# Kernel optimization log

Hardware: AMD Instinct MI355X
Metric: run time of the kernel (lower is better)

Reference implementation:

```python
import jax, jax.numpy as jnp
import numpy as np

B, DIM, HEADS, H, W = 4, 192, 6, 256, 256
C = DIM // HEADS  # channels per head
DN = ('NCHW', 'OIHW', 'NCHW')


def conv2d(x, w, b, padding='VALID', groups=1):
    y = jax.lax.conv_general_dilated(x, w, (1, 1), padding,
                                     dimension_numbers=DN,
                                     feature_group_count=groups)
    return y + b[None, :, None, None]


def setup_inputs() -> dict:
    key = jax.random.key(0)
    ks = jax.random.split(key, 8)
    s = 0.02
    return {
        'x': jax.random.normal(ks[0], (B, DIM, H, W), jnp.float32),
        'qkv_w': jax.random.normal(ks[1], (3 * DIM, DIM, 1, 1), jnp.float32) * s,
        'qkv_b': jnp.zeros((3 * DIM,), jnp.float32),
        'dw_w': jax.random.normal(ks[2], (3 * DIM, 1, 3, 3), jnp.float32) * s,
        'dw_b': jnp.zeros((3 * DIM,), jnp.float32),
        'proj_w': jax.random.normal(ks[3], (DIM, DIM, 1, 1), jnp.float32) * s,
        'proj_b': jnp.zeros((DIM,), jnp.float32),
        'temperature': jnp.ones((HEADS, 1, 1, 1), jnp.float32),
    }


def reference(x, qkv_w, qkv_b, dw_w, dw_b, proj_w, proj_b, temperature):
    # qkv projection: 1x1 conv then 3x3 depthwise conv
    qkv = conv2d(x, qkv_w, qkv_b)
    qkv = conv2d(qkv, dw_w, dw_b, padding='SAME', groups=3 * DIM)
    q, k, v = jnp.split(qkv, 3, axis=1)  # each (B, DIM, H, W)

    def heads(t):
        return t.reshape(B, HEADS, C, H, W)
    q, k, v = heads(q), heads(k), heads(v)

    # L2-normalize along W (matches F.normalize eps=1e-12)
    eps = 1e-12
    q = q / jnp.maximum(jnp.linalg.norm(q, axis=-1, keepdims=True), eps)
    k = k / jnp.maximum(jnp.linalg.norm(k, axis=-1, keepdims=True), eps)

    # per-channel HxH attention, contraction over W; temperature broadcasts over head
    attn = jnp.einsum('bncxw,bncyw->bncxy', q, k) * temperature  # (B,HEADS,C,H,H)
    attn = jax.nn.softmax(attn, axis=-1)
    out = jnp.einsum('bncxy,bncyw->bncxw', attn, v)  # (B,HEADS,C,H,W)

    out = out.reshape(B, DIM, H, W)
    return conv2d(out, proj_w, proj_b)
```

## Files before the change

### kernel.cpp

```cpp
#include <hip/hip_runtime.h>
#include <hip/hip_bf16.h>
#include <math.h>


#define HW 65536
#define IMW 256

typedef short bf16x8 __attribute__((ext_vector_type(8)));
typedef float f32x4  __attribute__((ext_vector_type(4)));

__device__ __forceinline__ float bf2f(ushort u) {
    return __uint_as_float((uint)u << 16);
}
__device__ __forceinline__ ushort f2bf(float f) {
    uint i = __float_as_uint(f);
    return (ushort)((i + 0x7FFFu + ((i >> 16) & 1u)) >> 16);
}

__global__ __launch_bounds__(256) void cvt_f32_bf16(const float* __restrict__ s,
                                                    ushort* __restrict__ d, int n)
{
    int i = blockIdx.x * 256 + threadIdx.x;
    if (i < n) d[i] = f2bf(s[i]);
}

__global__ __launch_bounds__(256) void cvt_transpose_f32(const float* __restrict__ src,
                                                         ushort* __restrict__ dst,
                                                         int R, int C,
                                                         long ssS, long ssD)
{
    __shared__ ushort Ls[64][72];
    int t = threadIdx.x;
    long z = blockIdx.z;
    src += z * ssS; dst += z * ssD;
    int c0 = blockIdx.x * 64, r0 = blockIdx.y * 64;
    {
        int r = t >> 2, cs = t & 3;
        const float* gp = src + (size_t)(r0 + r) * C + c0 + cs * 16;
        ushort tmp[16];
        #pragma unroll
        for (int q = 0; q < 4; ++q) {
            float4 v = *(const float4*)(gp + q * 4);
            tmp[q*4+0] = f2bf(v.x); tmp[q*4+1] = f2bf(v.y);
            tmp[q*4+2] = f2bf(v.z); tmp[q*4+3] = f2bf(v.w);
        }
        *(uint4*)&Ls[r][cs * 16]     = *(uint4*)&tmp[0];
        *(uint4*)&Ls[r][cs * 16 + 8] = *(uint4*)&tmp[8];
    }
    __syncthreads();
    {
        int cc = t & 63, seg = t >> 6;
        ushort tmp[16];
        #pragma unroll
        for (int j = 0; j < 16; ++j) tmp[j] = Ls[seg * 16 + j][cc];
        ushort* op = dst + (size_t)(c0 + cc) * R + r0 + seg * 16;
        *(uint4*)(op)     = *(uint4*)&tmp[0];
        *(uint4*)(op + 8) = *(uint4*)&tmp[8];
    }
}

__global__ __launch_bounds__(256) void transpose_bf16(const ushort* __restrict__ src,
                                                      ushort* __restrict__ dst,
                                                      int R, int C,
                                                      long ssS, long ssD)
{
    __shared__ ushort Ls[64][72];
    int t = threadIdx.x;
    long z = blockIdx.z;
    src += z * ssS; dst += z * ssD;
    int c0 = blockIdx.x * 64, r0 = blockIdx.y * 64;
    {
        int r = t >> 2, cs = t & 3;
        const ushort* gp = src + (size_t)(r0 + r) * C + c0 + cs * 16;
        *(uint4*)&Ls[r][cs * 16]     = *(const uint4*)(gp);
        *(uint4*)&Ls[r][cs * 16 + 8] = *(const uint4*)(gp + 8);
    }
    __syncthreads();
    {
        int cc = t & 63, seg = t >> 6;
        ushort tmp[16];
        #pragma unroll
        for (int j = 0; j < 16; ++j) tmp[j] = Ls[seg * 16 + j][cc];
        ushort* op = dst + (size_t)(c0 + cc) * R + r0 + seg * 16;
        *(uint4*)(op)     = *(uint4*)&tmp[0];
        *(uint4*)(op + 8) = *(uint4*)&tmp[8];
    }
}

__global__ __launch_bounds__(256) void transpose_v(const ushort* __restrict__ post,
                                                   ushort* __restrict__ vt)
{
    __shared__ ushort Ls[64][72];
    int t = threadIdx.x;
    int s = blockIdx.z;
    int b = s / 192, r = s - b * 192;
    const ushort* src = post + ((size_t)b * 576 + 384 + r) * HW;
    ushort*       dst = vt + (size_t)s * HW;
    int c0 = blockIdx.x * 64, r0 = blockIdx.y * 64;
    {
        int rr = t >> 2, cs = t & 3;
        const ushort* gp = src + (size_t)(r0 + rr) * IMW + c0 + cs * 16;
        *(uint4*)&Ls[rr][cs * 16]     = *(const uint4*)(gp);
        *(uint4*)&Ls[rr][cs * 16 + 8] = *(const uint4*)(gp + 8);
    }
    __syncthreads();
    {
        int cc = t & 63, seg = t >> 6;
        ushort tmp[16];
        #pragma unroll
        for (int j = 0; j < 16; ++j) tmp[j] = Ls[seg * 16 + j][cc];
        ushort* op = dst + (size_t)(c0 + cc) * IMW + r0 + seg * 16;
        *(uint4*)(op)     = *(uint4*)&tmp[0];
        *(uint4*)(op + 8) = *(uint4*)&tmp[8];
    }
}

__global__ __launch_bounds__(256) void gemm_mfma(const ushort* __restrict__ A, int lda, long sliceA,
                                                 const ushort* __restrict__ B, int ldb, long sliceB,
                                                 void* __restrict__ Dp, int ldd, long sliceD,
                                                 const float* __restrict__ bias,
                                                 int K, int outF32)
{
    __shared__ ushort Ws[64][40];
    __shared__ ushort Xs[256][40];
    int t = threadIdx.x, wv = t >> 6, lane = t & 63;
    long z = blockIdx.z;
    A += z * sliceA; B += z * sliceB;
    int m0 = blockIdx.x * 64, n0 = blockIdx.y * 256;

    f32x4 acc[16];
    #pragma unroll
    for (int i = 0; i < 16; ++i) acc[i] = (f32x4){0.f, 0.f, 0.f, 0.f};

    for (int k0 = 0; k0 < K; k0 += 32) {
        {   int r = t >> 2, s = t & 3;
            *(uint4*)&Ws[r][s * 8] =
                *(const uint4*)(A + (size_t)(m0 + r) * lda + k0 + s * 8);
        }
        {   const ushort* bp = B + (size_t)(n0 + t) * ldb + k0;
            #pragma unroll
            for (int s = 0; s < 4; ++s)
                *(uint4*)&Xs[t][s * 8] = *(const uint4*)(bp + s * 8);
        }
        __syncthreads();
        bf16x8 a = *(const bf16x8*)&Ws[wv * 16 + (lane & 15)][(lane >> 4) * 8];
        #pragma unroll
        for (int nt = 0; nt < 16; ++nt) {
            bf16x8 b = *(const bf16x8*)&Xs[nt * 16 + (lane & 15)][(lane >> 4) * 8];
            acc[nt] = __builtin_amdgcn_mfma_f32_16x16x32_bf16(a, b, acc[nt], 0, 0, 0);
        }
        __syncthreads();
    }

    int mrow = m0 + wv * 16 + (lane >> 4) * 4;
    int ncol = n0 + (lane & 15);
    if (outF32) {
        float* D = (float*)Dp + z * sliceD;
        #pragma unroll
        for (int r_ = 0; r_ < 4; ++r_) {
            float bv = bias ? bias[mrow + r_] : 0.f;
            #pragma unroll
            for (int nt = 0; nt < 16; ++nt)
                D[(size_t)(mrow + r_) * ldd + ncol + nt * 16] = acc[nt][r_] + bv;
        }
    } else {
        ushort* D = (ushort*)Dp + z * sliceD;
        #pragma unroll
        for (int r_ = 0; r_ < 4; ++r_) {
            float bv = bias ? bias[mrow + r_] : 0.f;
            #pragma unroll
            for (int nt = 0; nt < 16; ++nt)
                D[(size_t)(mrow + r_) * ldd + ncol + nt * 16] = f2bf(acc[nt][r_] + bv);
        }
    }
}

__global__ __launch_bounds__(256) void attn_fused(const ushort* __restrict__ post,
                                                  const ushort* __restrict__ vt,
                                                  const float* __restrict__ temp,
                                                  ushort* __restrict__ O)
{
    __shared__ ushort Ws[64][40];
    __shared__ ushort Xs[256][40];
    __shared__ ushort Ps[64][264];
    int t = threadIdx.x, wv = t >> 6, lane = t & 63;
    int s = blockIdx.y;
    int b = s / 192, ch = s - b * 192;
    const ushort* Aq = post + ((size_t)b * 576 + ch) * HW;
    const ushort* Bk = Aq + (size_t)192 * HW;
    const ushort* Vt = vt + (size_t)s * HW;
    int m0 = blockIdx.x * 64;

    f32x4 acc[16];
    #pragma unroll
    for (int i = 0; i < 16; ++i) acc[i] = (f32x4){0.f, 0.f, 0.f, 0.f};

    for (int k0 = 0; k0 < 256; k0 += 32) {
        {   int r = t >> 2, ss = t & 3;
            *(uint4*)&Ws[r][ss * 8] =
                *(const uint4*)(Aq + (size_t)(m0 + r) * IMW + k0 + ss * 8);
        }
        {   const ushort* bp = Bk + (size_t)t * IMW + k0;
            #pragma unroll
            for (int ss = 0; ss < 4; ++ss)
                *(uint4*)&Xs[t][ss * 8] = *(const uint4*)(bp + ss * 8);
        }
        __syncthreads();
        bf16x8 a = *(const bf16x8*)&Ws[wv * 16 + (lane & 15)][(lane >> 4) * 8];
        #pragma unroll
        for (int nt = 0; nt < 16; ++nt) {
            bf16x8 bfrag = *(const bf16x8*)&Xs[nt * 16 + (lane & 15)][(lane >> 4) * 8];
            acc[nt] = __builtin_amdgcn_mfma_f32_16x16x32_bf16(a, bfrag, acc[nt], 0, 0, 0);
        }
        __syncthreads();
    }

    float tv = temp[ch >> 5];
    #pragma unroll
    for (int r_ = 0; r_ < 4; ++r_) {
        float v[16];
        float mx = -3.4e38f;
        #pragma unroll
        for (int nt = 0; nt < 16; ++nt) { v[nt] = acc[nt][r_] * tv; mx = fmaxf(mx, v[nt]); }
        #pragma unroll
        for (int sh = 1; sh < 16; sh <<= 1) mx = fmaxf(mx, __shfl_xor(mx, sh, 64));
        float sum = 0.f;
        #pragma unroll
        for (int nt = 0; nt < 16; ++nt) { v[nt] = __expf(v[nt] - mx); sum += v[nt]; }
        #pragma unroll
        for (int sh = 1; sh < 16; sh <<= 1) sum += __shfl_xor(sum, sh, 64);
        float inv = 1.f / sum;
        int ml = wv * 16 + (lane >> 4) * 4 + r_;
        #pragma unroll
        for (int nt = 0; nt < 16; ++nt)
            Ps[ml][(lane & 15) + nt * 16] = f2bf(v[nt] * inv);
    }

    f32x4 acc2[16];
    #pragma unroll
    for (int i = 0; i < 16; ++i) acc2[i] = (f32x4){0.f, 0.f, 0.f, 0.f};

    for (int y0 = 0; y0 < 256; y0 += 32) {
        {   const ushort* bp = Vt + (size_t)t * IMW + y0;
            #pragma unroll
            for (int ss = 0; ss < 4; ++ss)
                *(uint4*)&Xs[t][ss * 8] = *(const uint4*)(bp + ss * 8);
        }
        __syncthreads();
        bf16x8 a = *(const bf16x8*)&Ps[wv * 16 + (lane & 15)][y0 + (lane >> 4) * 8];
        #pragma unroll
        for (int nt = 0; nt < 16; ++nt) {
            bf16x8 bfrag = *(const bf16x8*)&Xs[nt * 16 + (lane & 15)][(lane >> 4) * 8];
            acc2[nt] = __builtin_amdgcn_mfma_f32_16x16x32_bf16(a, bfrag, acc2[nt], 0, 0, 0);
        }
        __syncthreads();
    }

    ushort* Op = O + (size_t)s * HW;
    int mrow = m0 + wv * 16 + (lane >> 4) * 4;
    int ncol = lane & 15;
    #pragma unroll
    for (int r_ = 0; r_ < 4; ++r_) {
        #pragma unroll
        for (int nt = 0; nt < 16; ++nt)
            Op[(size_t)(mrow + r_) * IMW + ncol + nt * 16] = f2bf(acc2[nt][r_]);
    }
}

__global__ __launch_bounds__(256) void dw3x3_l2norm(const ushort* __restrict__ in,
                                                    const float* __restrict__ w,
                                                    const float* __restrict__ bias,
                                                    ushort* __restrict__ out)
{
    int t = threadIdx.x;
    int lane = t & 63, wv = t >> 6;
    int ch = blockIdx.y;
    int r0 = blockIdx.x * 16 + wv * 4;
    const ushort* img  = in  + ((size_t)blockIdx.z * 576 + ch) * HW;
    ushort*       outp = out + ((size_t)blockIdx.z * 576 + ch) * HW;
    int px = lane * 4;

    float rv[6][4], lv[6], rx[6];
    #pragma unroll
    for (int i = 0; i < 6; ++i) {
        int rr = r0 - 1 + i;
        if ((unsigned)rr <= 255u) {
            ushort4 cv = *(const ushort4*)&img[(size_t)rr * IMW + px];
            rv[i][0] = bf2f(cv.x); rv[i][1] = bf2f(cv.y);
            rv[i][2] = bf2f(cv.z); rv[i][3] = bf2f(cv.w);
        } else {
            rv[i][0] = rv[i][1] = rv[i][2] = rv[i][3] = 0.f;
        }
        float l = __shfl_up(rv[i][3], 1, 64);
        lv[i] = (lane == 0) ? 0.f : l;
        float r = __shfl_down(rv[i][0], 1, 64);
        rx[i] = (lane == 63) ? 0.f : r;
    }

    const float* wch = w + ch * 9;
    float bv = bias[ch];
    bool do_norm = (ch < 384);

    #pragma unroll
    for (int j = 0; j < 4; ++j) {
        float a0 = bv, a1 = bv, a2 = bv, a3 = bv;
        #pragma unroll
        for (int dy = 0; dy < 3; ++dy) {
            int i = j + dy;
            float w0 = wch[dy * 3], w1 = wch[dy * 3 + 1], w2 = wch[dy * 3 + 2];
            a0 += lv[i]    * w0 + rv[i][0] * w1 + rv[i][1] * w2;
            a1 += rv[i][0] * w0 + rv[i][1] * w1 + rv[i][2] * w2;
            a2 += rv[i][1] * w0 + rv[i][2] * w1 + rv[i][3] * w2;
            a3 += rv[i][2] * w0 + rv[i][3] * w1 + rx[i]    * w2;
        }
        if (do_norm) {
            float ss = a0 * a0 + a1 * a1 + a2 * a2 + a3 * a3;
            #pragma unroll
            for (int m = 1; m < 64; m <<= 1) ss += __shfl_xor(ss, m, 64);
            float inv = 1.0f / fmaxf(sqrtf(ss), 1e-12f);
            a0 *= inv; a1 *= inv; a2 *= inv; a3 *= inv;
        }
        ushort4 o;
        o.x = f2bf(a0); o.y = f2bf(a1); o.z = f2bf(a2); o.w = f2bf(a3);
        *(ushort4*)&outp[(size_t)(r0 + j) * IMW + px] = o;
    }
}

extern "C" void kernel_launch(void* const* d_in, const int* in_sizes, int n_in,
                              void* d_out, int out_size, void* d_ws, size_t ws_size,
                              hipStream_t stream)
{
    const float* x      = (const float*)d_in[0];
    const float* qkv_w  = (const float*)d_in[1];
    const float* qkv_b  = (const float*)d_in[2];
    const float* dw_w   = (const float*)d_in[3];
    const float* dw_b   = (const float*)d_in[4];
    const float* proj_w = (const float*)d_in[5];
    const float* proj_b = (const float*)d_in[6];
    const float* temp   = (const float*)d_in[7];
    float* out = (float*)d_out;

    const size_t off_wq   = 0;
    const size_t off_wp   = 110592;
    const size_t off_pre  = 262144;
    const size_t off_post = off_pre + (size_t)4 * 576 * HW;
    const size_t off_xt   = off_post + (size_t)4 * 576 * HW;
    const size_t total_us = off_xt + (size_t)4 * 192 * HW;
    if (ws_size < total_us * sizeof(ushort)) return;

    ushort* wsb  = (ushort*)d_ws;
    ushort* wq   = wsb + off_wq;
    ushort* wp   = wsb + off_wp;
    ushort* pre  = wsb + off_pre;
    ushort* post = wsb + off_post;
    ushort* xt   = wsb + off_xt;
    ushort* Obuf = pre;
    ushort* Otb  = pre + (size_t)4 * 192 * HW;

    const long SL = (long)192 * HW;

    cvt_f32_bf16<<<dim3(432), 256, 0, stream>>>(qkv_w, wq, 110592);
    cvt_f32_bf16<<<dim3(144), 256, 0, stream>>>(proj_w, wp, 36864);

    cvt_transpose_f32<<<dim3(1024, 3, 4), 256, 0, stream>>>(x, xt, 192, HW, SL, SL);
    gemm_mfma<<<dim3(9, 256, 4), 256, 0, stream>>>(wq, 192, 0, xt, 192, SL,
                                                   pre, HW, (long)576 * HW, qkv_b, 192, 0);
    dw3x3_l2norm<<<dim3(16, 576, 4), 256, 0, stream>>>(pre, dw_w, dw_b, post);
    transpose_v<<<dim3(4, 4, 768), 256, 0, stream>>>(post, xt);
    attn_fused<<<dim3(4, 768), 256, 0, stream>>>(post, xt, temp, Obuf);
    transpose_bf16<<<dim3(1024, 3, 4), 256, 0, stream>>>(Obuf, Otb, 192, HW, SL, SL);
    gemm_mfma<<<dim3(3, 256, 4), 256, 0, stream>>>(wp, 192, 0, Otb, 192, SL,
                                                   out, HW, SL, proj_b, 192, 1);
}
```

Baseline: 800.9 us.

## Prefetch GEMM tiles through registers with K=64 steps and XCD-aware block remap

The 1x1-conv GEMM now loads a K=64 slice per iteration and prefetches the next slice into registers while MFMAs run on the current LDS tile. This halves the barrier count and hides global load latency. Both the GEMM and the fused attention kernel switch to a 1D grid, remapped so that consecutive groups of 8 blocks share the same M tile or channel slice. The intent is better L2 locality across the chiplets. The larger LDS tiles and register prefetch buffers raise resource use and may reduce occupancy.

```diff
diff --git a/kernel.cpp b/kernel.cpp
--- a/kernel.cpp
+++ b/kernel.cpp
@@ -119,37 +119,65 @@
                                                  const ushort* __restrict__ B, int ldb, long sliceB,
                                                  void* __restrict__ Dp, int ldd, long sliceD,
                                                  const float* __restrict__ bias,
-                                                 int K, int outF32)
-{
-    __shared__ ushort Ws[64][40];
-    __shared__ ushort Xs[256][40];
+                                                 int K, int outF32, int NM, int NN)
+{
+    int lin = blockIdx.x;
+    int r8 = lin & 7, kk_ = lin >> 3;
+    int m = kk_ % NM, fg = kk_ / NM;
+    int g = fg * 8 + r8;
+    int nt_ = g % NN;
+    long z = g / NN;
+    int m0 = m * 64, n0 = nt_ * 256;
+
+    __shared__ ushort Ws[64][72];
+    __shared__ ushort Xs[256][72];
     int t = threadIdx.x, wv = t >> 6, lane = t & 63;
-    long z = blockIdx.z;
     A += z * sliceA; B += z * sliceB;
-    int m0 = blockIdx.x * 64, n0 = blockIdx.y * 256;
 
     f32x4 acc[16];
     #pragma unroll
     for (int i = 0; i < 16; ++i) acc[i] = (f32x4){0.f, 0.f, 0.f, 0.f};
 
-    for (int k0 = 0; k0 < K; k0 += 32) {
-        {   int r = t >> 2, s = t & 3;
-            *(uint4*)&Ws[r][s * 8] =
-                *(const uint4*)(A + (size_t)(m0 + r) * lda + k0 + s * 8);
-        }
-        {   const ushort* bp = B + (size_t)(n0 + t) * ldb + k0;
-            #pragma unroll
-            for (int s = 0; s < 4; ++s)
-                *(uint4*)&Xs[t][s * 8] = *(const uint4*)(bp + s * 8);
-        }
-        __syncthreads();
-        bf16x8 a = *(const bf16x8*)&Ws[wv * 16 + (lane & 15)][(lane >> 4) * 8];
-        #pragma unroll
-        for (int nt = 0; nt < 16; ++nt) {
-            bf16x8 b = *(const bf16x8*)&Xs[nt * 16 + (lane & 15)][(lane >> 4) * 8];
-            acc[nt] = __builtin_amdgcn_mfma_f32_16x16x32_bf16(a, b, acc[nt], 0, 0, 0);
-        }
-        __syncthreads();
+    const ushort* apg = A + (size_t)(m0 + (t >> 2)) * lda + (t & 3) * 16;
+    const ushort* bpg = B + (size_t)(n0 + t) * ldb;
+
+    uint4 ar[2], br[8];
+    ar[0] = *(const uint4*)(apg);
+    ar[1] = *(const uint4*)(apg + 8);
+    #pragma unroll
+    for (int c = 0; c < 8; ++c) br[c] = *(const uint4*)(bpg + c * 8);
+    *(uint4*)&Ws[t >> 2][(t & 3) * 16]     = ar[0];
+    *(uint4*)&Ws[t >> 2][(t & 3) * 16 + 8] = ar[1];
+    #pragma unroll
+    for (int c = 0; c < 8; ++c) *(uint4*)&Xs[t][c * 8] = br[c];
+    __syncthreads();
+
+    int nkit = K >> 6;
+    for (int kit = 0; kit < nkit; ++kit) {
+        if (kit + 1 < nkit) {
+            int ko = (kit + 1) * 64;
+            ar[0] = *(const uint4*)(apg + ko);
+            ar[1] = *(const uint4*)(apg + ko + 8);
+            #pragma unroll
+            for (int c = 0; c < 8; ++c) br[c] = *(const uint4*)(bpg + ko + c * 8);
+        }
+        #pragma unroll
+        for (int kk = 0; kk < 2; ++kk) {
+            bf16x8 a = *(const bf16x8*)&Ws[wv * 16 + (lane & 15)][kk * 32 + (lane >> 4) * 8];
+            #pragma unroll
+            for (int nt = 0; nt < 16; ++nt) {
+                bf16x8 b = *(const bf16x8*)&Xs[nt * 16 + (lane & 15)][kk * 32 + (lane >> 4) * 8];
+                acc[nt] = __builtin_amdgcn_mfma_f32_16x16x32_bf16(a, b, acc[nt], 0, 0, 0);
+            }
+        }
+        if (kit + 1 < nkit) {
+            __syncthreads();
+            *(uint4*)&Ws[t >> 2][(t & 3) * 16]     = ar[0];
+            *(uint4*)&Ws[t >> 2][(t & 3) * 16 + 8] = ar[1];
+            #pragma unroll
+            for (int c = 0; c < 8; ++c) *(uint4*)&Xs[t][c * 8] = br[c];
+            __syncthreads();
+        }
     }
 
     int mrow = m0 + wv * 16 + (lane >> 4) * 4;
@@ -184,12 +212,15 @@
     __shared__ ushort Xs[256][40];
     __shared__ ushort Ps[64][264];
     int t = threadIdx.x, wv = t >> 6, lane = t & 63;
-    int s = blockIdx.y;
+    int lin = blockIdx.x;
+    int r8 = lin & 7, k_ = lin >> 3;
+    int mtile = k_ & 3, fg = k_ >> 2;
+    int s = fg * 8 + r8;
     int b = s / 192, ch = s - b * 192;
     const ushort* Aq = post + ((size_t)b * 576 + ch) * HW;
     const ushort* Bk = Aq + (size_t)192 * HW;
     const ushort* Vt = vt + (size_t)s * HW;
-    int m0 = blockIdx.x * 64;
+    int m0 = mtile * 64;
 
     f32x4 acc[16];
     #pragma unroll
@@ -363,12 +394,14 @@
     cvt_f32_bf16<<<dim3(144), 256, 0, stream>>>(proj_w, wp, 36864);
 
     cvt_transpose_f32<<<dim3(1024, 3, 4), 256, 0, stream>>>(x, xt, 192, HW, SL, SL);
-    gemm_mfma<<<dim3(9, 256, 4), 256, 0, stream>>>(wq, 192, 0, xt, 192, SL,
-                                                   pre, HW, (long)576 * HW, qkv_b, 192, 0);
+    gemm_mfma<<<dim3(9 * 256 * 4), 256, 0, stream>>>(wq, 192, 0, xt, 192, SL,
+                                                     pre, HW, (long)576 * HW,
+                                                     qkv_b, 192, 0, 9, 256);
     dw3x3_l2norm<<<dim3(16, 576, 4), 256, 0, stream>>>(pre, dw_w, dw_b, post);
     transpose_v<<<dim3(4, 4, 768), 256, 0, stream>>>(post, xt);
-    attn_fused<<<dim3(4, 768), 256, 0, stream>>>(post, xt, temp, Obuf);
+    attn_fused<<<dim3(4 * 768), 256, 0, stream>>>(post, xt, temp, Obuf);
     transpose_bf16<<<dim3(1024, 3, 4), 256, 0, stream>>>(Obuf, Otb, 192, HW, SL, SL);
-    gemm_mfma<<<dim3(3, 256, 4), 256, 0, stream>>>(wp, 192, 0, Otb, 192, SL,
-                                                   out, HW, SL, proj_b, 192, 1);
-}
+    gemm_mfma<<<dim3(3 * 256 * 4), 256, 0, stream>>>(wp, 192, 0, Otb, 192, SL,
+                                                     out, HW, SL,
+                                                     proj_b, 192, 1, 3, 256);
+}
```

Measured after the change: 1.058 ms. 1.32x slower.
